# Optimization experiments

Hardware: AMD Instinct MI355X
Metric: run time of the kernel (lower is better)

The kernel has to match this reference:

```python
import jax, jax.numpy as jnp
import numpy as np

B, S, D = 8, 4096, 1024
N_LEVELS = 8
L = 8
EPS = 1e-3        # FSQ eps (bound shrink)
LN_EPS = 1e-5     # torch LayerNorm default eps


def setup_inputs() -> dict:
    key = jax.random.key(0)
    k1, k2 = jax.random.split(key)
    regrs = jax.random.normal(k1, (B, S, D), dtype=jnp.float32)
    ln_w = jnp.ones((D,), dtype=jnp.float32)
    ln_b = jnp.zeros((D,), dtype=jnp.float32)
    # nn.Linear(d_model, n_levels, bias=False): weight shape [n_levels, d_model]
    W = jax.random.normal(k2, (N_LEVELS, D), dtype=jnp.float32) * (1.0 / np.sqrt(D))
    return {"regrs": regrs, "ln_w": ln_w, "ln_b": ln_b, "W": W}


def reference(regrs, ln_w, ln_b, W):
    # LayerNorm over last dim (biased variance, matching torch)
    mean = jnp.mean(regrs, axis=-1, keepdims=True)
    var = jnp.mean(jnp.square(regrs - mean), axis=-1, keepdims=True)
    x = (regrs - mean) * jax.lax.rsqrt(var + LN_EPS) * ln_w + ln_b
    # skinny projection to n_levels channels
    z = jnp.einsum('bsd,nd->bsn', x, W)  # [B,S,N_LEVELS]
    half_l = L * (1.0 - EPS) / 2.0
    bounded = half_l * jnp.tanh(z)
    # round with straight-through estimator
    code = bounded + jax.lax.stop_gradient(jnp.round(bounded) - bounded)
    return code
```

## Files before the change

kernel.cpp:

```cpp
#include <hip/hip_runtime.h>
#include <math.h>

#define NLEV 8
#define D_DIM 1024

struct TB  { float  t[8]; };
struct TBD { double t[8]; };

template<int CTRL>
__device__ __forceinline__ float ror_add(float v) {
    int r = __builtin_amdgcn_update_dpp(0, __float_as_int(v), CTRL, 0xF, 0xF, true);
    return v + __int_as_float(r);
}
__device__ __forceinline__ float red16(float v) {
    v = ror_add<0x121>(v);
    v = ror_add<0x122>(v);
    v = ror_add<0x124>(v);
    v = ror_add<0x128>(v);
    return v;
}
__device__ __forceinline__ float wave_allreduce(float v) {
    v = red16(v);
    v += __shfl_xor(v, 16, 64);
    v += __shfl_xor(v, 32, 64);
    return v;
}

__global__ __launch_bounds__(512) void fsq_fused(
        const float* __restrict__ xg,
        const float* __restrict__ gg,
        const float* __restrict__ bg,
        const float* __restrict__ Wg,
        float* __restrict__ outg,
        int nrows, TB tb, TBD tbd)
{
    __shared__ float Vs[NLEV][D_DIM];
    __shared__ float redc1[8][NLEV];
    __shared__ float redc0[8][NLEV];

    const int tid  = (int)threadIdx.x;
    const int lane = tid & 63;
    const int wv   = tid >> 6;

    {
        const int col = tid * 2;
        const float2 g2 = *(const float2*)(gg + col);
        const float2 b2 = *(const float2*)(bg + col);
        float pc1[NLEV], pc0[NLEV];
        #pragma unroll
        for (int n = 0; n < NLEV; ++n) {
            const float2 w2 = *(const float2*)(Wg + n * D_DIM + col);
            float2 v2;
            v2.x = g2.x * w2.x; v2.y = g2.y * w2.y;
            *(float2*)&Vs[n][col] = v2;
            pc1[n] = v2.x + v2.y;
            pc0[n] = b2.x * w2.x + b2.y * w2.y;
        }
        #pragma unroll
        for (int n = 0; n < NLEV; ++n) {
            pc1[n] = wave_allreduce(pc1[n]);
            pc0[n] = wave_allreduce(pc0[n]);
        }
        if (lane == 0) {
            #pragma unroll
            for (int n = 0; n < NLEV; ++n) { redc1[wv][n] = pc1[n]; redc0[wv][n] = pc0[n]; }
        }
    }
    __syncthreads();
    const int nsel = lane & 7;
    float C1sel = 0.f, C0sel = 0.f;
    #pragma unroll
    for (int w = 0; w < 8; ++w) { C1sel += redc1[w][nsel]; C0sel += redc0[w][nsel]; }

    const long wave_row0 = (long)blockIdx.x * 32 + (long)wv * 4;
    const float4* xb = (const float4*)xg;

    for (int p = 0; p < 4; ++p) {
        const long row = wave_row0 + p;
        if (row >= nrows) break;

        const float4* xr = xb + row * (D_DIM / 4);
        float4 xv0 = xr[lane];
        float4 xv1 = xr[64 + lane];
        float4 xv2 = xr[128 + lane];
        float4 xv3 = xr[192 + lane];

        float s = 0.f, sq = 0.f;
        float acc[NLEV];
        #pragma unroll
        for (int n = 0; n < NLEV; ++n) acc[n] = 0.f;

        #pragma unroll
        for (int j = 0; j < 4; ++j) {
            const float4 a = (j == 0) ? xv0 : (j == 1) ? xv1 : (j == 2) ? xv2 : xv3;
            const int vcol = j * 256 + lane * 4;
            s += (a.x + a.y) + (a.z + a.w);
            sq = fmaf(a.x, a.x, sq); sq = fmaf(a.y, a.y, sq);
            sq = fmaf(a.z, a.z, sq); sq = fmaf(a.w, a.w, sq);
            #pragma unroll
            for (int n = 0; n < NLEV; ++n) {
                const float4 v4 = *(const float4*)&Vs[n][vcol];
                acc[n] = fmaf(a.x, v4.x, acc[n]);
                acc[n] = fmaf(a.y, v4.y, acc[n]);
                acc[n] = fmaf(a.z, v4.z, acc[n]);
                acc[n] = fmaf(a.w, v4.w, acc[n]);
            }
        }

        s = red16(s); sq = red16(sq);
        #pragma unroll
        for (int n = 0; n < NLEV; ++n) acc[n] = red16(acc[n]);

        float u0 = (lane & 4) ? acc[4] : acc[0];
        float u1 = (lane & 4) ? acc[5] : acc[1];
        float u2 = (lane & 4) ? acc[6] : acc[2];
        float u3 = (lane & 4) ? acc[7] : acc[3];
        float w0 = (lane & 2) ? u2 : u0;
        float w1 = (lane & 2) ? u3 : u1;
        float Ssel = (lane & 1) ? w1 : w0;

        Ssel += __shfl_xor(Ssel, 16, 64); Ssel += __shfl_xor(Ssel, 32, 64);
        s    += __shfl_xor(s, 16, 64);    s    += __shfl_xor(s, 32, 64);
        sq   += __shfl_xor(sq, 16, 64);   sq   += __shfl_xor(sq, 32, 64);

        bool flag = false;
        int  cnt_fast = 0;
        if (lane < NLEV) {
            const float mean = s * (1.0f / 1024.0f);
            const float var  = sq * (1.0f / 1024.0f) - mean * mean;
            const float rstd = 1.0f / sqrtf(var + 1e-5f);
            const float z = rstd * (Ssel - mean * C1sel) + C0sel;
            float mind = 1e30f;
            #pragma unroll
            for (int k = 0; k < 8; ++k) {
                cnt_fast += (z > tb.t[k]) ? 1 : 0;
                mind = fminf(mind, fabsf(z - tb.t[k]));
            }
            flag = (mind < 1.0e-3f);
        }
        const unsigned long long bal = __ballot(flag);

        if (bal == 0ULL) {
            if (lane < NLEV) outg[row * NLEV + lane] = (float)(cnt_fast - 4);
        } else {
            double ds = 0.0, dsq = 0.0;
            #pragma unroll
            for (int j = 0; j < 4; ++j) {
                const float4 a = (j == 0) ? xv0 : (j == 1) ? xv1 : (j == 2) ? xv2 : xv3;
                const double x0 = (double)a.x, x1 = (double)a.y;
                const double x2 = (double)a.z, x3 = (double)a.w;
                ds += ((x0 + x1) + (x2 + x3));
                dsq = fma(x0, x0, dsq); dsq = fma(x1, x1, dsq);
                dsq = fma(x2, x2, dsq); dsq = fma(x3, x3, dsq);
            }
            #pragma unroll
            for (int off = 32; off >= 1; off >>= 1) {
                ds  += __shfl_xor(ds, off, 64);
                dsq += __shfl_xor(dsq, off, 64);
            }
            const double mean = ds * (1.0 / 1024.0);
            const double var  = dsq * (1.0 / 1024.0) - mean * mean;
            const double rstd = 1.0 / sqrt(var + 1e-5);

            double dacc[NLEV];
            #pragma unroll
            for (int n = 0; n < NLEV; ++n) dacc[n] = 0.0;
            #pragma unroll
            for (int j = 0; j < 4; ++j) {
                const int col = j * 256 + lane * 4;
                const float4 a = (j == 0) ? xv0 : (j == 1) ? xv1 : (j == 2) ? xv2 : xv3;
                const float4 g4 = *(const float4*)(gg + col);
                const float4 b4 = *(const float4*)(bg + col);
                const double y0 = fma(((double)a.x - mean) * rstd, (double)g4.x, (double)b4.x);
                const double y1 = fma(((double)a.y - mean) * rstd, (double)g4.y, (double)b4.y);
                const double y2 = fma(((double)a.z - mean) * rstd, (double)g4.z, (double)b4.z);
                const double y3 = fma(((double)a.w - mean) * rstd, (double)g4.w, (double)b4.w);
                #pragma unroll
                for (int n = 0; n < NLEV; ++n) {
                    const float4 w4 = *(const float4*)(Wg + n * D_DIM + col);
                    dacc[n] = fma(y0, (double)w4.x, dacc[n]);
                    dacc[n] = fma(y1, (double)w4.y, dacc[n]);
                    dacc[n] = fma(y2, (double)w4.z, dacc[n]);
                    dacc[n] = fma(y3, (double)w4.w, dacc[n]);
                }
            }
            #pragma unroll
            for (int off = 32; off >= 1; off >>= 1) {
                #pragma unroll
                for (int n = 0; n < NLEV; ++n) dacc[n] += __shfl_xor(dacc[n], off, 64);
            }
            if (lane < NLEV) {
                double a0 = (lane & 4) ? dacc[4] : dacc[0];
                double a1 = (lane & 4) ? dacc[5] : dacc[1];
                double a2 = (lane & 4) ? dacc[6] : dacc[2];
                double a3 = (lane & 4) ? dacc[7] : dacc[3];
                double b0 = (lane & 2) ? a2 : a0;
                double b1 = (lane & 2) ? a3 : a1;
                const double z = (lane & 1) ? b1 : b0;
                int c = 0;
                #pragma unroll
                for (int k = 0; k < 8; ++k) c += (z > tbd.t[k]) ? 1 : 0;
                outg[row * NLEV + lane] = (float)(c - 4);
            }
        }
    }
}

extern "C" void kernel_launch(void* const* d_in, const int* in_sizes, int n_in,
                              void* d_out, int out_size, void* d_ws, size_t ws_size,
                              hipStream_t stream) {
    (void)n_in; (void)out_size; (void)d_ws; (void)ws_size;
    const float* regrs = (const float*)d_in[0];
    const float* ln_w  = (const float*)d_in[1];
    const float* ln_b  = (const float*)d_in[2];
    const float* W     = (const float*)d_in[3];
    float* out = (float*)d_out;

    const int nrows = in_sizes[0] / D_DIM;
    const int nblocks = (nrows + 31) / 32;

    TB tb; TBD tbd;
    for (int k = 0; k < 8; ++k) {
        const double y = ((double)k - 3.5) / 3.996;
        tbd.t[k] = atanh(y);
        tb.t[k]  = (float)tbd.t[k];
    }

    fsq_fused<<<nblocks, 512, 0, stream>>>(regrs, ln_w, ln_b, W, out, nrows, tb, tbd);
}
```

Before: 215.4 us.

## Process two rows per wave iteration to reuse LDS weight loads

```diff
diff --git a/kernel.cpp b/kernel.cpp
--- a/kernel.cpp
+++ b/kernel.cpp
@@ -26,7 +26,97 @@
     return v;
 }
 
-__global__ __launch_bounds__(512) void fsq_fused(
+__device__ __forceinline__ void repair_row(
+        long row, float4 a0, float4 a1, float4 a2, float4 a3,
+        const float* __restrict__ gg, const float* __restrict__ bg,
+        const float* __restrict__ Wg, float* __restrict__ outg,
+        const TBD& tbd, int lane)
+{
+    double ds = 0.0, dsq = 0.0;
+    #pragma unroll
+    for (int j = 0; j < 4; ++j) {
+        const float4 a = (j == 0) ? a0 : (j == 1) ? a1 : (j == 2) ? a2 : a3;
+        const double x0 = (double)a.x, x1 = (double)a.y;
+        const double x2 = (double)a.z, x3 = (double)a.w;
+        ds += ((x0 + x1) + (x2 + x3));
+        dsq = fma(x0, x0, dsq); dsq = fma(x1, x1, dsq);
+        dsq = fma(x2, x2, dsq); dsq = fma(x3, x3, dsq);
+    }
+    #pragma unroll
+    for (int off = 32; off >= 1; off >>= 1) {
+        ds  += __shfl_xor(ds, off, 64);
+        dsq += __shfl_xor(dsq, off, 64);
+    }
+    const double mean = ds * (1.0 / 1024.0);
+    const double var  = dsq * (1.0 / 1024.0) - mean * mean;
+    const double rstd = 1.0 / sqrt(var + 1e-5);
+
+    double dacc[NLEV];
+    #pragma unroll
+    for (int n = 0; n < NLEV; ++n) dacc[n] = 0.0;
+    #pragma unroll
+    for (int j = 0; j < 4; ++j) {
+        const int col = j * 256 + lane * 4;
+        const float4 a = (j == 0) ? a0 : (j == 1) ? a1 : (j == 2) ? a2 : a3;
+        const float4 g4 = *(const float4*)(gg + col);
+        const float4 b4 = *(const float4*)(bg + col);
+        const double y0 = fma(((double)a.x - mean) * rstd, (double)g4.x, (double)b4.x);
+        const double y1 = fma(((double)a.y - mean) * rstd, (double)g4.y, (double)b4.y);
+        const double y2 = fma(((double)a.z - mean) * rstd, (double)g4.z, (double)b4.z);
+        const double y3 = fma(((double)a.w - mean) * rstd, (double)g4.w, (double)b4.w);
+        #pragma unroll
+        for (int n = 0; n < NLEV; ++n) {
+            const float4 w4 = *(const float4*)(Wg + n * D_DIM + col);
+            dacc[n] = fma(y0, (double)w4.x, dacc[n]);
+            dacc[n] = fma(y1, (double)w4.y, dacc[n]);
+            dacc[n] = fma(y2, (double)w4.z, dacc[n]);
+            dacc[n] = fma(y3, (double)w4.w, dacc[n]);
+        }
+    }
+    #pragma unroll
+    for (int off = 32; off >= 1; off >>= 1) {
+        #pragma unroll
+        for (int n = 0; n < NLEV; ++n) dacc[n] += __shfl_xor(dacc[n], off, 64);
+    }
+    if (lane < NLEV) {
+        double a0d = (lane & 4) ? dacc[4] : dacc[0];
+        double a1d = (lane & 4) ? dacc[5] : dacc[1];
+        double a2d = (lane & 4) ? dacc[6] : dacc[2];
+        double a3d = (lane & 4) ? dacc[7] : dacc[3];
+        double b0d = (lane & 2) ? a2d : a0d;
+        double b1d = (lane & 2) ? a3d : a1d;
+        const double z = (lane & 1) ? b1d : b0d;
+        int c = 0;
+        #pragma unroll
+        for (int k = 0; k < 8; ++k) c += (z > tbd.t[k]) ? 1 : 0;
+        outg[row * NLEV + lane] = (float)(c - 4);
+    }
+}
+
+__device__ __forceinline__ bool fast_epilogue(
+        long row, float s, float sq, float Ssel, float C1sel, float C0sel,
+        float* __restrict__ outg, const TB& tb, int lane)
+{
+    bool flag = false;
+    if (lane < NLEV) {
+        const float mean = s * (1.0f / 1024.0f);
+        const float var  = sq * (1.0f / 1024.0f) - mean * mean;
+        const float rstd = 1.0f / sqrtf(var + 1e-5f);
+        const float z = rstd * (Ssel - mean * C1sel) + C0sel;
+        int cnt = 0;
+        float mind = 1e30f;
+        #pragma unroll
+        for (int k = 0; k < 8; ++k) {
+            cnt += (z > tb.t[k]) ? 1 : 0;
+            mind = fminf(mind, fabsf(z - tb.t[k]));
+        }
+        outg[row * NLEV + lane] = (float)(cnt - 4);
+        flag = (mind < 1.0e-3f);
+    }
+    return flag;
+}
+
+__global__ __launch_bounds__(512, 4) void fsq_fused(
         const float* __restrict__ xg,
         const float* __restrict__ gg,
         const float* __restrict__ bg,
@@ -72,137 +162,92 @@
     #pragma unroll
     for (int w = 0; w < 8; ++w) { C1sel += redc1[w][nsel]; C0sel += redc0[w][nsel]; }
 
-    const long wave_row0 = (long)blockIdx.x * 32 + (long)wv * 4;
+    const long wave_row0 = (long)blockIdx.x * 64 + (long)wv * 8;
     const float4* xb = (const float4*)xg;
 
     for (int p = 0; p < 4; ++p) {
-        const long row = wave_row0 + p;
-        if (row >= nrows) break;
-
-        const float4* xr = xb + row * (D_DIM / 4);
-        float4 xv0 = xr[lane];
-        float4 xv1 = xr[64 + lane];
-        float4 xv2 = xr[128 + lane];
-        float4 xv3 = xr[192 + lane];
-
-        float s = 0.f, sq = 0.f;
-        float acc[NLEV];
-        #pragma unroll
-        for (int n = 0; n < NLEV; ++n) acc[n] = 0.f;
+        const long r0 = wave_row0 + 2 * p;
+        if (r0 >= nrows) break;
+        const long r1 = r0 + 1;
+        const bool has1 = (r1 < nrows);
+
+        const float4* xr0 = xb + r0 * (D_DIM / 4);
+        const float4* xr1 = xb + (has1 ? r1 : r0) * (D_DIM / 4);
+        float4 a0 = xr0[lane];
+        float4 a1 = xr0[64 + lane];
+        float4 a2 = xr0[128 + lane];
+        float4 a3 = xr0[192 + lane];
+        float4 b0 = xr1[lane];
+        float4 b1 = xr1[64 + lane];
+        float4 b2 = xr1[128 + lane];
+        float4 b3 = xr1[192 + lane];
+
+        float s0 = 0.f, sq0 = 0.f, s1 = 0.f, sq1 = 0.f;
+        float acc0[NLEV], acc1[NLEV];
+        #pragma unroll
+        for (int n = 0; n < NLEV; ++n) { acc0[n] = 0.f; acc1[n] = 0.f; }
 
         #pragma unroll
         for (int j = 0; j < 4; ++j) {
-            const float4 a = (j == 0) ? xv0 : (j == 1) ? xv1 : (j == 2) ? xv2 : xv3;
+            const float4 xa = (j == 0) ? a0 : (j == 1) ? a1 : (j == 2) ? a2 : a3;
+            const float4 xc = (j == 0) ? b0 : (j == 1) ? b1 : (j == 2) ? b2 : b3;
             const int vcol = j * 256 + lane * 4;
-            s += (a.x + a.y) + (a.z + a.w);
-            sq = fmaf(a.x, a.x, sq); sq = fmaf(a.y, a.y, sq);
-            sq = fmaf(a.z, a.z, sq); sq = fmaf(a.w, a.w, sq);
+            s0 += (xa.x + xa.y) + (xa.z + xa.w);
+            sq0 = fmaf(xa.x, xa.x, sq0); sq0 = fmaf(xa.y, xa.y, sq0);
+            sq0 = fmaf(xa.z, xa.z, sq0); sq0 = fmaf(xa.w, xa.w, sq0);
+            s1 += (xc.x + xc.y) + (xc.z + xc.w);
+            sq1 = fmaf(xc.x, xc.x, sq1); sq1 = fmaf(xc.y, xc.y, sq1);
+            sq1 = fmaf(xc.z, xc.z, sq1); sq1 = fmaf(xc.w, xc.w, sq1);
             #pragma unroll
             for (int n = 0; n < NLEV; ++n) {
                 const float4 v4 = *(const float4*)&Vs[n][vcol];
-                acc[n] = fmaf(a.x, v4.x, acc[n]);
-                acc[n] = fmaf(a.y, v4.y, acc[n]);
-                acc[n] = fmaf(a.z, v4.z, acc[n]);
-                acc[n] = fmaf(a.w, v4.w, acc[n]);
+                acc0[n] = fmaf(xa.x, v4.x, acc0[n]);
+                acc0[n] = fmaf(xa.y, v4.y, acc0[n]);
+                acc0[n] = fmaf(xa.z, v4.z, acc0[n]);
+                acc0[n] = fmaf(xa.w, v4.w, acc0[n]);
+                acc1[n] = fmaf(xc.x, v4.x, acc1[n]);
+                acc1[n] = fmaf(xc.y, v4.y, acc1[n]);
+                acc1[n] = fmaf(xc.z, v4.z, acc1[n]);
+                acc1[n] = fmaf(xc.w, v4.w, acc1[n]);
             }
         }
 
-        s = red16(s); sq = red16(sq);
-        #pragma unroll
-        for (int n = 0; n < NLEV; ++n) acc[n] = red16(acc[n]);
-
-        float u0 = (lane & 4) ? acc[4] : acc[0];
-        float u1 = (lane & 4) ? acc[5] : acc[1];
-        float u2 = (lane & 4) ? acc[6] : acc[2];
-        float u3 = (lane & 4) ? acc[7] : acc[3];
-        float w0 = (lane & 2) ? u2 : u0;
-        float w1 = (lane & 2) ? u3 : u1;
-        float Ssel = (lane & 1) ? w1 : w0;
-
-        Ssel += __shfl_xor(Ssel, 16, 64); Ssel += __shfl_xor(Ssel, 32, 64);
-        s    += __shfl_xor(s, 16, 64);    s    += __shfl_xor(s, 32, 64);
-        sq   += __shfl_xor(sq, 16, 64);   sq   += __shfl_xor(sq, 32, 64);
-
-        bool flag = false;
-        int  cnt_fast = 0;
-        if (lane < NLEV) {
-            const float mean = s * (1.0f / 1024.0f);
-            const float var  = sq * (1.0f / 1024.0f) - mean * mean;
-            const float rstd = 1.0f / sqrtf(var + 1e-5f);
-            const float z = rstd * (Ssel - mean * C1sel) + C0sel;
-            float mind = 1e30f;
-            #pragma unroll
-            for (int k = 0; k < 8; ++k) {
-                cnt_fast += (z > tb.t[k]) ? 1 : 0;
-                mind = fminf(mind, fabsf(z - tb.t[k]));
-            }
-            flag = (mind < 1.0e-3f);
-        }
-        const unsigned long long bal = __ballot(flag);
-
-        if (bal == 0ULL) {
-            if (lane < NLEV) outg[row * NLEV + lane] = (float)(cnt_fast - 4);
-        } else {
-            double ds = 0.0, dsq = 0.0;
-            #pragma unroll
-            for (int j = 0; j < 4; ++j) {
-                const float4 a = (j == 0) ? xv0 : (j == 1) ? xv1 : (j == 2) ? xv2 : xv3;
-                const double x0 = (double)a.x, x1 = (double)a.y;
-                const double x2 = (double)a.z, x3 = (double)a.w;
-                ds += ((x0 + x1) + (x2 + x3));
-                dsq = fma(x0, x0, dsq); dsq = fma(x1, x1, dsq);
-                dsq = fma(x2, x2, dsq); dsq = fma(x3, x3, dsq);
-            }
-            #pragma unroll
-            for (int off = 32; off >= 1; off >>= 1) {
-                ds  += __shfl_xor(ds, off, 64);
-                dsq += __shfl_xor(dsq, off, 64);
-            }
-            const double mean = ds * (1.0 / 1024.0);
-            const double var  = dsq * (1.0 / 1024.0) - mean * mean;
-            const double rstd = 1.0 / sqrt(var + 1e-5);
-
-            double dacc[NLEV];
-            #pragma unroll
-            for (int n = 0; n < NLEV; ++n) dacc[n] = 0.0;
-            #pragma unroll
-            for (int j = 0; j < 4; ++j) {
-                const int col = j * 256 + lane * 4;
-                const float4 a = (j == 0) ? xv0 : (j == 1) ? xv1 : (j == 2) ? xv2 : xv3;
-                const float4 g4 = *(const float4*)(gg + col);
-                const float4 b4 = *(const float4*)(bg + col);
-                const double y0 = fma(((double)a.x - mean) * rstd, (double)g4.x, (double)b4.x);
-                const double y1 = fma(((double)a.y - mean) * rstd, (double)g4.y, (double)b4.y);
-                const double y2 = fma(((double)a.z - mean) * rstd, (double)g4.z, (double)b4.z);
-                const double y3 = fma(((double)a.w - mean) * rstd, (double)g4.w, (double)b4.w);
-                #pragma unroll
-                for (int n = 0; n < NLEV; ++n) {
-                    const float4 w4 = *(const float4*)(Wg + n * D_DIM + col);
-                    dacc[n] = fma(y0, (double)w4.x, dacc[n]);
-                    dacc[n] = fma(y1, (double)w4.y, dacc[n]);
-                    dacc[n] = fma(y2, (double)w4.z, dacc[n]);
-                    dacc[n] = fma(y3, (double)w4.w, dacc[n]);
-                }
-            }
-            #pragma unroll
-            for (int off = 32; off >= 1; off >>= 1) {
-                #pragma unroll
-                for (int n = 0; n < NLEV; ++n) dacc[n] += __shfl_xor(dacc[n], off, 64);
-            }
-            if (lane < NLEV) {
-                double a0 = (lane & 4) ? dacc[4] : dacc[0];
-                double a1 = (lane & 4) ? dacc[5] : dacc[1];
-                double a2 = (lane & 4) ? dacc[6] : dacc[2];
-                double a3 = (lane & 4) ? dacc[7] : dacc[3];
-                double b0 = (lane & 2) ? a2 : a0;
-                double b1 = (lane & 2) ? a3 : a1;
-                const double z = (lane & 1) ? b1 : b0;
-                int c = 0;
-                #pragma unroll
-                for (int k = 0; k < 8; ++k) c += (z > tbd.t[k]) ? 1 : 0;
-                outg[row * NLEV + lane] = (float)(c - 4);
-            }
-        }
+        s0 = red16(s0); sq0 = red16(sq0);
+        s1 = red16(s1); sq1 = red16(sq1);
+        #pragma unroll
+        for (int n = 0; n < NLEV; ++n) { acc0[n] = red16(acc0[n]); acc1[n] = red16(acc1[n]); }
+
+        float u00 = (lane & 4) ? acc0[4] : acc0[0];
+        float u01 = (lane & 4) ? acc0[5] : acc0[1];
+        float u02 = (lane & 4) ? acc0[6] : acc0[2];
+        float u03 = (lane & 4) ? acc0[7] : acc0[3];
+        float w00 = (lane & 2) ? u02 : u00;
+        float w01 = (lane & 2) ? u03 : u01;
+        float Ssel0 = (lane & 1) ? w01 : w00;
+
+        float u10 = (lane & 4) ? acc1[4] : acc1[0];
+        float u11 = (lane & 4) ? acc1[5] : acc1[1];
+        float u12 = (lane & 4) ? acc1[6] : acc1[2];
+        float u13 = (lane & 4) ? acc1[7] : acc1[3];
+        float w10 = (lane & 2) ? u12 : u10;
+        float w11 = (lane & 2) ? u13 : u11;
+        float Ssel1 = (lane & 1) ? w11 : w10;
+
+        Ssel0 += __shfl_xor(Ssel0, 16, 64); Ssel0 += __shfl_xor(Ssel0, 32, 64);
+        Ssel1 += __shfl_xor(Ssel1, 16, 64); Ssel1 += __shfl_xor(Ssel1, 32, 64);
+        s0    += __shfl_xor(s0, 16, 64);    s0    += __shfl_xor(s0, 32, 64);
+        sq0   += __shfl_xor(sq0, 16, 64);   sq0   += __shfl_xor(sq0, 32, 64);
+        s1    += __shfl_xor(s1, 16, 64);    s1    += __shfl_xor(s1, 32, 64);
+        sq1   += __shfl_xor(sq1, 16, 64);   sq1   += __shfl_xor(sq1, 32, 64);
+
+        const bool flag0 = fast_epilogue(r0, s0, sq0, Ssel0, C1sel, C0sel, outg, tb, lane);
+        const bool flag1 = has1 ? fast_epilogue(r1, s1, sq1, Ssel1, C1sel, C0sel, outg, tb, lane)
+                                : false;
+
+        const unsigned long long bal0 = __ballot(flag0);
+        const unsigned long long bal1 = __ballot(flag1);
+        if (bal0 != 0ULL)          repair_row(r0, a0, a1, a2, a3, gg, bg, Wg, outg, tbd, lane);
+        if (bal1 != 0ULL && has1)  repair_row(r1, b0, b1, b2, b3, gg, bg, Wg, outg, tbd, lane);
     }
 }
 
@@ -217,7 +262,7 @@
     float* out = (float*)d_out;
 
     const int nrows = in_sizes[0] / D_DIM;
-    const int nblocks = (nrows + 31) / 32;
+    const int nblocks = (nrows + 63) / 64;
 
     TB tb; TBD tbd;
     for (int k = 0; k < 8; ++k) {
```

Measured after the change: 230.0 us. +6.8%, slower.

## Prefetch next row, defer fp64 repair rows, process eight rows per wave

Applied to the files above, without the earlier changes.

```diff
diff --git a/kernel.cpp b/kernel.cpp
--- a/kernel.cpp
+++ b/kernel.cpp
@@ -26,7 +26,103 @@
     return v;
 }
 
-__global__ __launch_bounds__(512) void fsq_fused(
+__device__ __forceinline__ void repair_row_reload(
+        long row, const float* __restrict__ xg,
+        const float* __restrict__ gg, const float* __restrict__ bg,
+        const float* __restrict__ Wg, float* __restrict__ outg,
+        const TBD& tbd, int lane)
+{
+    const float4* xb4 = (const float4*)(xg + row * D_DIM);
+    const float4 x0 = xb4[lane];
+    const float4 x1 = xb4[64 + lane];
+    const float4 x2 = xb4[128 + lane];
+    const float4 x3 = xb4[192 + lane];
+
+    double ds = 0.0, dsq = 0.0;
+    #pragma unroll
+    for (int j = 0; j < 4; ++j) {
+        const float4 a = (j == 0) ? x0 : (j == 1) ? x1 : (j == 2) ? x2 : x3;
+        const double v0 = (double)a.x, v1 = (double)a.y;
+        const double v2 = (double)a.z, v3 = (double)a.w;
+        ds += ((v0 + v1) + (v2 + v3));
+        dsq = fma(v0, v0, dsq); dsq = fma(v1, v1, dsq);
+        dsq = fma(v2, v2, dsq); dsq = fma(v3, v3, dsq);
+    }
+    #pragma unroll
+    for (int off = 32; off >= 1; off >>= 1) {
+        ds  += __shfl_xor(ds, off, 64);
+        dsq += __shfl_xor(dsq, off, 64);
+    }
+    const double mean = ds * (1.0 / 1024.0);
+    const double var  = dsq * (1.0 / 1024.0) - mean * mean;
+    const double rstd = 1.0 / sqrt(var + 1e-5);
+
+    double dacc[NLEV];
+    #pragma unroll
+    for (int n = 0; n < NLEV; ++n) dacc[n] = 0.0;
+    #pragma unroll
+    for (int j = 0; j < 4; ++j) {
+        const int col = j * 256 + lane * 4;
+        const float4 a = (j == 0) ? x0 : (j == 1) ? x1 : (j == 2) ? x2 : x3;
+        const float4 g4 = *(const float4*)(gg + col);
+        const float4 b4 = *(const float4*)(bg + col);
+        const double y0 = fma(((double)a.x - mean) * rstd, (double)g4.x, (double)b4.x);
+        const double y1 = fma(((double)a.y - mean) * rstd, (double)g4.y, (double)b4.y);
+        const double y2 = fma(((double)a.z - mean) * rstd, (double)g4.z, (double)b4.z);
+        const double y3 = fma(((double)a.w - mean) * rstd, (double)g4.w, (double)b4.w);
+        #pragma unroll
+        for (int n = 0; n < NLEV; ++n) {
+            const float4 w4 = *(const float4*)(Wg + n * D_DIM + col);
+            dacc[n] = fma(y0, (double)w4.x, dacc[n]);
+            dacc[n] = fma(y1, (double)w4.y, dacc[n]);
+            dacc[n] = fma(y2, (double)w4.z, dacc[n]);
+            dacc[n] = fma(y3, (double)w4.w, dacc[n]);
+        }
+    }
+    #pragma unroll
+    for (int off = 32; off >= 1; off >>= 1) {
+        #pragma unroll
+        for (int n = 0; n < NLEV; ++n) dacc[n] += __shfl_xor(dacc[n], off, 64);
+    }
+    if (lane < NLEV) {
+        double a0d = (lane & 4) ? dacc[4] : dacc[0];
+        double a1d = (lane & 4) ? dacc[5] : dacc[1];
+        double a2d = (lane & 4) ? dacc[6] : dacc[2];
+        double a3d = (lane & 4) ? dacc[7] : dacc[3];
+        double b0d = (lane & 2) ? a2d : a0d;
+        double b1d = (lane & 2) ? a3d : a1d;
+        const double z = (lane & 1) ? b1d : b0d;
+        int c = 0;
+        #pragma unroll
+        for (int k = 0; k < 8; ++k) c += (z > tbd.t[k]) ? 1 : 0;
+        outg[row * NLEV + lane] = (float)(c - 4);
+    }
+}
+
+__device__ __forceinline__ bool fast_epilogue(
+        long row, float s, float sq, float Ssel, float C1sel, float C0sel,
+        float* __restrict__ outg, const TB& tb, int lane)
+{
+    bool flag = false;
+    if (lane < NLEV) {
+        const float mean = s * (1.0f / 1024.0f);
+        const float var  = sq * (1.0f / 1024.0f) - mean * mean;
+        const float rstd = 1.0f / sqrtf(var + 1e-5f);
+        const float z = rstd * (Ssel - mean * C1sel) + C0sel;
+        int cnt = 0;
+        float mind = 1e30f;
+        #pragma unroll
+        for (int k = 0; k < 8; ++k) {
+            cnt += (z > tb.t[k]) ? 1 : 0;
+            mind = fminf(mind, fabsf(z - tb.t[k]));
+        }
+        outg[row * NLEV + lane] = (float)(cnt - 4);
+        flag = (mind < 1.0e-3f);
+    }
+    return flag;
+}
+
+__global__ __launch_bounds__(512, 2) void fsq_fused(
         const float* __restrict__ xg,
         const float* __restrict__ gg,
         const float* __restrict__ bg,
@@ -72,18 +168,29 @@
     #pragma unroll
     for (int w = 0; w < 8; ++w) { C1sel += redc1[w][nsel]; C0sel += redc0[w][nsel]; }
 
-    const long wave_row0 = (long)blockIdx.x * 32 + (long)wv * 4;
+    const long wave_row0 = (long)blockIdx.x * 64 + (long)wv * 8;
     const float4* xb = (const float4*)xg;
-
-    for (int p = 0; p < 4; ++p) {
+    const long last = (long)nrows - 1;
+
+    float4 c0, c1, c2, c3;
+    {
+        const long r = (wave_row0 <= last) ? wave_row0 : last;
+        const float4* pr = xb + r * (D_DIM / 4);
+        c0 = pr[lane]; c1 = pr[64 + lane]; c2 = pr[128 + lane]; c3 = pr[192 + lane];
+    }
+
+    unsigned rmask = 0u;
+
+    #pragma unroll
+    for (int p = 0; p < 8; ++p) {
         const long row = wave_row0 + p;
-        if (row >= nrows) break;
-
-        const float4* xr = xb + row * (D_DIM / 4);
-        float4 xv0 = xr[lane];
-        float4 xv1 = xr[64 + lane];
-        float4 xv2 = xr[128 + lane];
-        float4 xv3 = xr[192 + lane];
+
+        float4 n0, n1, n2, n3;
+        if (p < 7) {
+            const long rn = (row + 1 <= last) ? row + 1 : last;
+            const float4* pr = xb + rn * (D_DIM / 4);
+            n0 = pr[lane]; n1 = pr[64 + lane]; n2 = pr[128 + lane]; n3 = pr[192 + lane];
+        }
 
         float s = 0.f, sq = 0.f;
         float acc[NLEV];
@@ -92,7 +199,7 @@
 
         #pragma unroll
         for (int j = 0; j < 4; ++j) {
-            const float4 a = (j == 0) ? xv0 : (j == 1) ? xv1 : (j == 2) ? xv2 : xv3;
+            const float4 a = (j == 0) ? c0 : (j == 1) ? c1 : (j == 2) ? c2 : c3;
             const int vcol = j * 256 + lane * 4;
             s += (a.x + a.y) + (a.z + a.w);
             sq = fmaf(a.x, a.x, sq); sq = fmaf(a.y, a.y, sq);
@@ -123,86 +230,18 @@
         s    += __shfl_xor(s, 16, 64);    s    += __shfl_xor(s, 32, 64);
         sq   += __shfl_xor(sq, 16, 64);   sq   += __shfl_xor(sq, 32, 64);
 
-        bool flag = false;
-        int  cnt_fast = 0;
-        if (lane < NLEV) {
-            const float mean = s * (1.0f / 1024.0f);
-            const float var  = sq * (1.0f / 1024.0f) - mean * mean;
-            const float rstd = 1.0f / sqrtf(var + 1e-5f);
-            const float z = rstd * (Ssel - mean * C1sel) + C0sel;
-            float mind = 1e30f;
-            #pragma unroll
-            for (int k = 0; k < 8; ++k) {
-                cnt_fast += (z > tb.t[k]) ? 1 : 0;
-                mind = fminf(mind, fabsf(z - tb.t[k]));
-            }
-            flag = (mind < 1.0e-3f);
-        }
-        const unsigned long long bal = __ballot(flag);
-
-        if (bal == 0ULL) {
-            if (lane < NLEV) outg[row * NLEV + lane] = (float)(cnt_fast - 4);
-        } else {
-            double ds = 0.0, dsq = 0.0;
-            #pragma unroll
-            for (int j = 0; j < 4; ++j) {
-                const float4 a = (j == 0) ? xv0 : (j == 1) ? xv1 : (j == 2) ? xv2 : xv3;
-                const double x0 = (double)a.x, x1 = (double)a.y;
-                const double x2 = (double)a.z, x3 = (double)a.w;
-                ds += ((x0 + x1) + (x2 + x3));
-                dsq = fma(x0, x0, dsq); dsq = fma(x1, x1, dsq);
-                dsq = fma(x2, x2, dsq); dsq = fma(x3, x3, dsq);
-            }
-            #pragma unroll
-            for (int off = 32; off >= 1; off >>= 1) {
-                ds  += __shfl_xor(ds, off, 64);
-                dsq += __shfl_xor(dsq, off, 64);
-            }
-            const double mean = ds * (1.0 / 1024.0);
-            const double var  = dsq * (1.0 / 1024.0) - mean * mean;
-            const double rstd = 1.0 / sqrt(var + 1e-5);
-
-            double dacc[NLEV];
-            #pragma unroll
-            for (int n = 0; n < NLEV; ++n) dacc[n] = 0.0;
-            #pragma unroll
-            for (int j = 0; j < 4; ++j) {
-                const int col = j * 256 + lane * 4;
-                const float4 a = (j == 0) ? xv0 : (j == 1) ? xv1 : (j == 2) ? xv2 : xv3;
-                const float4 g4 = *(const float4*)(gg + col);
-                const float4 b4 = *(const float4*)(bg + col);
-                const double y0 = fma(((double)a.x - mean) * rstd, (double)g4.x, (double)b4.x);
-                const double y1 = fma(((double)a.y - mean) * rstd, (double)g4.y, (double)b4.y);
-                const double y2 = fma(((double)a.z - mean) * rstd, (double)g4.z, (double)b4.z);
-                const double y3 = fma(((double)a.w - mean) * rstd, (double)g4.w, (double)b4.w);
-                #pragma unroll
-                for (int n = 0; n < NLEV; ++n) {
-                    const float4 w4 = *(const float4*)(Wg + n * D_DIM + col);
-                    dacc[n] = fma(y0, (double)w4.x, dacc[n]);
-                    dacc[n] = fma(y1, (double)w4.y, dacc[n]);
-                    dacc[n] = fma(y2, (double)w4.z, dacc[n]);
-                    dacc[n] = fma(y3, (double)w4.w, dacc[n]);
-                }
-            }
-            #pragma unroll
-            for (int off = 32; off >= 1; off >>= 1) {
-                #pragma unroll
-                for (int n = 0; n < NLEV; ++n) dacc[n] += __shfl_xor(dacc[n], off, 64);
-            }
-            if (lane < NLEV) {
-                double a0 = (lane & 4) ? dacc[4] : dacc[0];
-                double a1 = (lane & 4) ? dacc[5] : dacc[1];
-                double a2 = (lane & 4) ? dacc[6] : dacc[2];
-                double a3 = (lane & 4) ? dacc[7] : dacc[3];
-                double b0 = (lane & 2) ? a2 : a0;
-                double b1 = (lane & 2) ? a3 : a1;
-                const double z = (lane & 1) ? b1 : b0;
-                int c = 0;
-                #pragma unroll
-                for (int k = 0; k < 8; ++k) c += (z > tbd.t[k]) ? 1 : 0;
-                outg[row * NLEV + lane] = (float)(c - 4);
-            }
-        }
+        const bool flag = (row < (long)nrows)
+                        ? fast_epilogue(row, s, sq, Ssel, C1sel, C0sel, outg, tb, lane)
+                        : false;
+        if (__ballot(flag) != 0ULL) rmask |= (1u << p);
+
+        if (p < 7) { c0 = n0; c1 = n1; c2 = n2; c3 = n3; }
+    }
+
+    while (rmask) {
+        const int p = __builtin_ctz(rmask);
+        rmask &= rmask - 1u;
+        repair_row_reload(wave_row0 + p, xg, gg, bg, Wg, outg, tbd, lane);
     }
 }
 
@@ -217,7 +256,7 @@
     float* out = (float*)d_out;
 
     const int nrows = in_sizes[0] / D_DIM;
-    const int nblocks = (nrows + 31) / 32;
+    const int nblocks = (nrows + 63) / 64;
 
     TB tb; TBD tbd;
     for (int k = 0; k < 8; ++k) {
```

New measurement: 269.9 us. 1.25x slower.
